# Kernel optimization log

Measured on AMD Instinct MI355X. Metric: run time of the kernel, lower is better.

Reference implementation:

```python
import jax, jax.numpy as jnp
import numpy as np

N_NODES = 100000
N_EDGES = 1200000
NUM_GRAPHS = 64
D_IN = 64
D_H = 64
D_OUT = 2
BN_EPS = 1e-5


def setup_inputs() -> dict:
    key = jax.random.key(0)
    ks = jax.random.split(key, 12)
    x = jax.random.normal(ks[0], (N_NODES, D_IN), dtype=jnp.float32)
    edge_index = jax.random.randint(ks[1], (2, N_EDGES), 0, N_NODES, dtype=jnp.int64 if jax.config.read('jax_enable_x64') else jnp.int32)
    batch = jnp.sort(jax.random.randint(ks[2], (N_NODES,), 0, NUM_GRAPHS))
    s = 1.0 / np.sqrt(D_H)
    W1 = jax.random.uniform(ks[3], (D_IN, D_H), minval=-s, maxval=s, dtype=jnp.float32)
    b1 = jnp.zeros((D_H,), jnp.float32)
    g1 = jnp.ones((D_H,), jnp.float32); be1 = jnp.zeros((D_H,), jnp.float32)
    m1 = jax.random.normal(ks[4], (D_H,), dtype=jnp.float32) * 0.1
    v1 = jax.random.uniform(ks[5], (D_H,), minval=0.5, maxval=1.5, dtype=jnp.float32)
    W2 = jax.random.uniform(ks[6], (D_H, D_H), minval=-s, maxval=s, dtype=jnp.float32)
    b2 = jnp.zeros((D_H,), jnp.float32)
    g2 = jnp.ones((D_H,), jnp.float32); be2 = jnp.zeros((D_H,), jnp.float32)
    m2 = jax.random.normal(ks[7], (D_H,), dtype=jnp.float32) * 0.1
    v2 = jax.random.uniform(ks[8], (D_H,), minval=0.5, maxval=1.5, dtype=jnp.float32)
    Wc = jax.random.uniform(ks[9], (D_H, D_OUT), minval=-s, maxval=s, dtype=jnp.float32)
    bc = jnp.zeros((D_OUT,), jnp.float32)
    return dict(x=x, edge_index=edge_index, batch=batch, W1=W1, b1=b1, g1=g1, be1=be1, m1=m1, v1=v1,
                W2=W2, b2=b2, g2=g2, be2=be2, m2=m2, v2=v2, Wc=Wc, bc=bc)


def _gcn_conv(x, src, dst, W, b):
    n = x.shape[0]
    h = x @ W  # [N, Dh]
    deg = jax.ops.segment_sum(jnp.ones_like(dst, dtype=h.dtype), dst, num_segments=n)  # includes self-loops
    dinv = jax.lax.rsqrt(jnp.maximum(deg, 1.0))
    norm = dinv[src] * dinv[dst]  # [E+N]
    msg = h[src] * norm[:, None]
    out = jax.ops.segment_sum(msg, dst, num_segments=n)
    return out + b


def _bn(x, g, be, m, v):
    return (x - m) * (g * jax.lax.rsqrt(v + BN_EPS)) + be


def reference(x, edge_index, batch, W1, b1, g1, be1, m1, v1, W2, b2, g2, be2, m2, v2, Wc, bc):
    n = x.shape[0]
    loop = jnp.arange(n, dtype=edge_index.dtype)
    src = jnp.concatenate([edge_index[0], loop])
    dst = jnp.concatenate([edge_index[1], loop])
    h = _gcn_conv(x, src, dst, W1, b1)
    h = jax.nn.relu(_bn(h, g1, be1, m1, v1))  # dropout is identity in eval
    h = _gcn_conv(h, src, dst, W2, b2)
    h = jax.nn.relu(_bn(h, g2, be2, m2, v2))
    # global mean pool over graphs
    sums = jax.ops.segment_sum(h, batch, num_segments=NUM_GRAPHS)
    cnts = jax.ops.segment_sum(jnp.ones((n,), h.dtype), batch, num_segments=NUM_GRAPHS)
    pooled = sums / jnp.maximum(cnts, 1.0)[:, None]
    return pooled @ Wc + bc
```

## Files before the change

kernel.cpp:

```cpp
#include <hip/hip_runtime.h>

#define N_NODES_C 100000
#define N_EDGES_C 1200000
#define NUM_GRAPHS_C 64
#define D_C 64
#define CAP_C 64
#define NPASS_C 8
#define BN_EPS_C 1e-5f

typedef unsigned short u16;
typedef unsigned int u32;

using frag_ab = __attribute__((ext_vector_type(8))) short;
using f32x4   = __attribute__((ext_vector_type(4))) float;

__device__ __forceinline__ u16 f2bf(float f) {
    u32 x = __float_as_uint(f);
    x += 0x7fffu + ((x >> 16) & 1u);
    return (u16)(x >> 16);
}
__device__ __forceinline__ float bf2f(u16 u) {
    return __uint_as_float(((u32)u) << 16);
}

__global__ void k_prep(const float* __restrict__ x,
                       const float* __restrict__ W1, const float* __restrict__ W2,
                       u16* __restrict__ Xb, u16* __restrict__ Wb1,
                       u16* __restrict__ Wb2, u16* __restrict__ T) {
    int i = blockIdx.x * 256 + threadIdx.x;
    int base = i * 4;
    if (base < N_NODES_C * D_C) {
        float4 f = *(const float4*)(x + base);
        ushort4 o;
        o.x = f2bf(f.x); o.y = f2bf(f.y); o.z = f2bf(f.z); o.w = f2bf(f.w);
        *(ushort4*)(Xb + base) = o;
    }
    if (i < 4096) {
        int n = i >> 6, k = i & 63;
        Wb1[i] = f2bf(W1[k * 64 + n]);
        Wb2[i] = f2bf(W2[k * 64 + n]);
    }
    if (i < 64) T[(size_t)N_NODES_C * 64 + i] = 0;
}

__global__ void __launch_bounds__(256) k_scatter(
        const int* __restrict__ src, const int* __restrict__ dst,
        int* __restrict__ cnt, int* __restrict__ col) {
    int pass = blockIdx.x & (NPASS_C - 1);
    int chunk = blockIdx.x >> 3;
    int nchunks = gridDim.x >> 3;
    const int RANGE = N_NODES_C / NPASS_C;
    int lo = pass * RANGE;
    int hi = (pass == NPASS_C - 1) ? N_NODES_C : lo + RANGE;
    const int nquads = N_EDGES_C / 4;
    int tid = chunk * 256 + threadIdx.x;
    int nthreads = nchunks * 256;
    const int4* dst4 = (const int4*)dst;
    const int4* src4 = (const int4*)src;
    for (int i = tid; i < nquads; i += nthreads) {
        int4 d4 = dst4[i];
        int dd[4] = {d4.x, d4.y, d4.z, d4.w};
        bool in0 = dd[0] >= lo && dd[0] < hi;
        bool in1 = dd[1] >= lo && dd[1] < hi;
        bool in2 = dd[2] >= lo && dd[2] < hi;
        bool in3 = dd[3] >= lo && dd[3] < hi;
        if (in0 | in1 | in2 | in3) {
            int4 s4 = src4[i];
            int ss[4] = {s4.x, s4.y, s4.z, s4.w};
            bool in[4] = {in0, in1, in2, in3};
#pragma unroll
            for (int k = 0; k < 4; ++k) {
                if (in[k]) {
                    int pos = atomicAdd(&cnt[dd[k]], 1);
                    if (pos < CAP_C) col[(size_t)dd[k] * CAP_C + pos] = ss[k];
                }
            }
        }
    }
}

__global__ void __launch_bounds__(256) k_gemm_mfma(
        const u16* __restrict__ Xb, const u16* __restrict__ Wb,
        const int* __restrict__ cnt, u16* __restrict__ T) {
    int lane = threadIdx.x & 63;
    int q = lane >> 4, ln = lane & 15;
    int wave = blockIdx.x * 4 + (threadIdx.x >> 6);
    int nwaves = gridDim.x * 4;
    frag_ab bfr[4][2];
#pragma unroll
    for (int nt = 0; nt < 4; ++nt)
#pragma unroll
        for (int kh = 0; kh < 2; ++kh)
            bfr[nt][kh] = *(const frag_ab*)(Wb + (nt * 16 + ln) * 64 + kh * 32 + q * 8);
    const int nstrips = N_NODES_C / 16;
    for (int s = wave; s < nstrips; s += nwaves) {
        int r0 = s * 16;
        frag_ab a0 = *(const frag_ab*)(Xb + (size_t)(r0 + ln) * 64 + q * 8);
        frag_ab a1 = *(const frag_ab*)(Xb + (size_t)(r0 + ln) * 64 + 32 + q * 8);
        f32x4 acc[4];
#pragma unroll
        for (int nt = 0; nt < 4; ++nt) {
            acc[nt] = (f32x4){0.f, 0.f, 0.f, 0.f};
            acc[nt] = __builtin_amdgcn_mfma_f32_16x16x32_bf16(a0, bfr[nt][0], acc[nt], 0, 0, 0);
            acc[nt] = __builtin_amdgcn_mfma_f32_16x16x32_bf16(a1, bfr[nt][1], acc[nt], 0, 0, 0);
        }
        float di[4];
#pragma unroll
        for (int reg = 0; reg < 4; ++reg)
            di[reg] = rsqrtf((float)(cnt[r0 + q * 4 + reg] + 1));
#pragma unroll
        for (int nt = 0; nt < 4; ++nt)
#pragma unroll
            for (int reg = 0; reg < 4; ++reg)
                T[(size_t)(r0 + q * 4 + reg) * 64 + nt * 16 + ln] =
                    f2bf(acc[nt][reg] * di[reg]);
    }
}

template <bool POOL>
__device__ __forceinline__ void gather_body(
        const u16* __restrict__ T, const int* __restrict__ col,
        const int* __restrict__ cnt,
        const float* __restrict__ b, const float* __restrict__ g,
        const float* __restrict__ be, const float* __restrict__ m,
        const float* __restrict__ v, const int* __restrict__ batch,
        u16* __restrict__ Ab, float* __restrict__ pooled) {
    const int ZROW = N_NODES_C;
    int lane = threadIdx.x & 63;
    int h = lane >> 4, c = lane & 15;
    int cbase = c << 2;
    int wave = blockIdx.x * 4 + (threadIdx.x >> 6);
    int nwaves = gridDim.x * 4;
    float scv[4], c0v[4];
#pragma unroll
    for (int i = 0; i < 4; ++i) {
        float sci = g[cbase + i] * rsqrtf(v[cbase + i] + BN_EPS_C);
        scv[i] = sci;
        c0v[i] = (b[cbase + i] - m[cbase + i]) * sci + be[cbase + i];
    }
    const int chunk = (N_NODES_C + nwaves - 1) / nwaves;
    int p0 = wave * chunk;
    int p1 = p0 + chunk; if (p1 > N_NODES_C) p1 = N_NODES_C;
    if (p0 >= p1) return;

    float psum = 0.f; int curg = -1;

    int dRaw = cnt[p0];
    int cvRaw = col[((size_t)(u32)p0 << 6) + lane];

    for (int p = p0; p < p1; ++p) {
        int deg = __builtin_amdgcn_readfirstlane(dRaw);
        if (deg > 63) deg = 63;
        int cvR = cvRaw;
        if (p + 1 < p1) {
            dRaw = cnt[p + 1];
            cvRaw = col[((size_t)(u32)(p + 1) << 6) + lane];
        }
        int cv = (lane < deg) ? cvR : ((lane == deg) ? p : ZROW);
        int iters = (deg + 4) >> 2;
        float a0 = 0.f, a1 = 0.f, a2 = 0.f, a3 = 0.f;
        int sl = h;
        int j = 0;
        for (; j + 2 <= iters; j += 2) {
            int i0 = __shfl(cv, sl);
            int i1 = __shfl(cv, sl + 4);
            uint2 t0 = *(const uint2*)(T + (((size_t)(u32)i0) << 6) + (c << 2));
            uint2 t1 = *(const uint2*)(T + (((size_t)(u32)i1) << 6) + (c << 2));
            a0 += __uint_as_float(t0.x << 16); a1 += __uint_as_float(t0.x & 0xffff0000u);
            a2 += __uint_as_float(t0.y << 16); a3 += __uint_as_float(t0.y & 0xffff0000u);
            a0 += __uint_as_float(t1.x << 16); a1 += __uint_as_float(t1.x & 0xffff0000u);
            a2 += __uint_as_float(t1.y << 16); a3 += __uint_as_float(t1.y & 0xffff0000u);
            sl += 8;
        }
        if (j < iters) {
            int i0 = __shfl(cv, sl);
            uint2 t0 = *(const uint2*)(T + (((size_t)(u32)i0) << 6) + (c << 2));
            a0 += __uint_as_float(t0.x << 16); a1 += __uint_as_float(t0.x & 0xffff0000u);
            a2 += __uint_as_float(t0.y << 16); a3 += __uint_as_float(t0.y & 0xffff0000u);
        }
        a0 += __shfl_xor(a0, 16); a0 += __shfl_xor(a0, 32);
        a1 += __shfl_xor(a1, 16); a1 += __shfl_xor(a1, 32);
        a2 += __shfl_xor(a2, 16); a2 += __shfl_xor(a2, 32);
        a3 += __shfl_xor(a3, 16); a3 += __shfl_xor(a3, 32);
        float dr = rsqrtf((float)(deg + 1));
        if (POOL) {
            float asel = (h & 2) ? ((h & 1) ? a3 : a2) : ((h & 1) ? a1 : a0);
            float scl  = (h & 2) ? ((h & 1) ? scv[3] : scv[2]) : ((h & 1) ? scv[1] : scv[0]);
            float c0l  = (h & 2) ? ((h & 1) ? c0v[3] : c0v[2]) : ((h & 1) ? c0v[1] : c0v[0]);
            float vh = fmaxf(fmaf(asel * dr, scl, c0l), 0.f);
            int gg = batch[p];
            if (gg != curg) {
                if (curg >= 0) atomicAdd(&pooled[curg * 64 + cbase + h], psum);
                curg = gg; psum = 0.f;
            }
            psum += vh;
        } else {
            float v0 = fmaxf(fmaf(a0 * dr, scv[0], c0v[0]), 0.f);
            float v1 = fmaxf(fmaf(a1 * dr, scv[1], c0v[1]), 0.f);
            float v2 = fmaxf(fmaf(a2 * dr, scv[2], c0v[2]), 0.f);
            float v3 = fmaxf(fmaf(a3 * dr, scv[3], c0v[3]), 0.f);
            if (h == 0) {
                u32 w0 = (u32)f2bf(v0) | ((u32)f2bf(v1) << 16);
                u32 w1 = (u32)f2bf(v2) | ((u32)f2bf(v3) << 16);
                *(uint2*)(Ab + (((size_t)(u32)p) << 6) + (c << 2)) = make_uint2(w0, w1);
            }
        }
    }
    if (POOL && curg >= 0) atomicAdd(&pooled[curg * 64 + cbase + h], psum);
}

__global__ void __launch_bounds__(256) k_gather1(
        const u16* __restrict__ T, const int* __restrict__ col,
        const int* __restrict__ cnt,
        const float* __restrict__ b, const float* __restrict__ g,
        const float* __restrict__ be, const float* __restrict__ m,
        const float* __restrict__ v, u16* __restrict__ Ab) {
    gather_body<false>(T, col, cnt, b, g, be, m, v, nullptr, Ab, nullptr);
}

__global__ void __launch_bounds__(256) k_gather2(
        const u16* __restrict__ T, const int* __restrict__ col,
        const int* __restrict__ cnt,
        const float* __restrict__ b, const float* __restrict__ g,
        const float* __restrict__ be, const float* __restrict__ m,
        const float* __restrict__ v, const int* __restrict__ batch,
        float* __restrict__ pooled) {
    gather_body<true>(T, col, cnt, b, g, be, m, v, batch, nullptr, pooled);
}

__global__ void k_final(const float* __restrict__ pooled, const int* __restrict__ batch,
                        const float* __restrict__ Wc, const float* __restrict__ bc,
                        float* __restrict__ out) {
    __shared__ float sp[64 * 65];
    __shared__ int sub[64];
    int t = threadIdx.x;
    for (int i = t; i < 4096; i += 256) sp[(i >> 6) * 65 + (i & 63)] = pooled[i];
    if (t < 64) {
        int lo = 0, hi = N_NODES_C;
        while (lo < hi) { int mid = (lo + hi) >> 1; if (batch[mid] > t) hi = mid; else lo = mid + 1; }
        sub[t] = lo;
    }
    __syncthreads();
    if (t < 64) {
        int gi = t;
        int lb = gi ? sub[gi - 1] : 0;
        int cntg = sub[gi] - lb;
        float inv = 1.0f / fmaxf((float)cntg, 1.0f);
        float a0 = 0.f, a1 = 0.f;
#pragma unroll 8
        for (int f = 0; f < 64; ++f) {
            float p = sp[gi * 65 + f];
            a0 = fmaf(p, Wc[f * 2 + 0], a0);
            a1 = fmaf(p, Wc[f * 2 + 1], a1);
        }
        out[gi * 2 + 0] = a0 * inv + bc[0];
        out[gi * 2 + 1] = a1 * inv + bc[1];
    }
}

extern "C" void kernel_launch(void* const* d_in, const int* in_sizes, int n_in,
                              void* d_out, int out_size, void* d_ws, size_t ws_size,
                              hipStream_t stream) {
    const float* x    = (const float*)d_in[0];
    const int*   ei   = (const int*)d_in[1];
    const int*   batch= (const int*)d_in[2];
    const float* W1 = (const float*)d_in[3];
    const float* b1 = (const float*)d_in[4];
    const float* g1 = (const float*)d_in[5];
    const float* be1= (const float*)d_in[6];
    const float* m1 = (const float*)d_in[7];
    const float* v1 = (const float*)d_in[8];
    const float* W2 = (const float*)d_in[9];
    const float* b2 = (const float*)d_in[10];
    const float* g2 = (const float*)d_in[11];
    const float* be2= (const float*)d_in[12];
    const float* m2 = (const float*)d_in[13];
    const float* v2 = (const float*)d_in[14];
    const float* Wc = (const float*)d_in[15];
    const float* bc = (const float*)d_in[16];
    float* out = (float*)d_out;

    char* ws = (char*)d_ws;
    size_t off = 0;
    auto alloc = [&](size_t bytes) {
        size_t o = off;
        off = (off + bytes + 511) & ~(size_t)511;
        return o;
    };
    size_t o_cnt   = alloc((size_t)N_NODES_C * 4);
    size_t o_pool  = alloc((size_t)NUM_GRAPHS_C * D_C * 4);
    size_t zero_bytes = off;
    size_t o_col   = alloc((size_t)N_NODES_C * CAP_C * 4);
    size_t o_xb    = alloc((size_t)N_NODES_C * D_C * 2);
    size_t o_wb1   = alloc(4096 * 2);
    size_t o_wb2   = alloc(4096 * 2);
    size_t o_t     = alloc((size_t)(N_NODES_C + 1) * D_C * 2);
    size_t o_ab    = alloc((size_t)N_NODES_C * D_C * 2);
    (void)ws_size; (void)in_sizes; (void)n_in; (void)out_size;

    int*   cnt    = (int*)(ws + o_cnt);
    float* pooled = (float*)(ws + o_pool);
    int*   col    = (int*)(ws + o_col);
    u16*   Xb     = (u16*)(ws + o_xb);
    u16*   Wb1    = (u16*)(ws + o_wb1);
    u16*   Wb2    = (u16*)(ws + o_wb2);
    u16*   T      = (u16*)(ws + o_t);
    u16*   Ab     = (u16*)(ws + o_ab);

    const int* srcp = ei;
    const int* dstp = ei + N_EDGES_C;

    hipMemsetAsync(ws, 0, zero_bytes, stream);

    int pblocks = (N_NODES_C * D_C / 4 + 255) / 256;
    int sblocks = 2048;
    int gblocks = 2048;
    int mblocks = 1563;
    k_prep<<<pblocks, 256, 0, stream>>>(x, W1, W2, Xb, Wb1, Wb2, T);
    k_scatter<<<sblocks, 256, 0, stream>>>(srcp, dstp, cnt, col);

    k_gemm_mfma<<<mblocks, 256, 0, stream>>>(Xb, Wb1, cnt, T);
    k_gather1<<<gblocks, 256, 0, stream>>>(T, col, cnt, b1, g1, be1, m1, v1, Ab);
    k_gemm_mfma<<<mblocks, 256, 0, stream>>>(Ab, Wb2, cnt, T);
    k_gather2<<<gblocks, 256, 0, stream>>>(T, col, cnt, b2, g2, be2, m2, v2,
                                           batch, pooled);
    k_final<<<1, 256, 0, stream>>>(pooled, batch, Wc, bc, out);
}
```

Baseline: 253.8 us.

## Replace fixed-capacity adjacency buckets with exact CSR built by count-scan-place

Swaps the padded per-node column buckets (64 slots each) for a compact CSR layout. Degrees and per-edge slot positions are counted with atomics in the prep kernel, a three-kernel prefix scan gives row starts, and a placement kernel writes sources without atomics. Gather kernels read neighbour lists from the CSR offsets, which shrinks the column array and makes reads contiguous. In exchange it adds three scan launches plus the pos array traffic, and the placement step still does scattered writes.

```diff
diff --git a/kernel.cpp b/kernel.cpp
--- a/kernel.cpp
+++ b/kernel.cpp
@@ -4,9 +4,9 @@
 #define N_EDGES_C 1200000
 #define NUM_GRAPHS_C 64
 #define D_C 64
-#define CAP_C 64
 #define NPASS_C 8
 #define BN_EPS_C 1e-5f
+#define SCAN_B 391
 
 typedef unsigned short u16;
 typedef unsigned int u32;
@@ -25,8 +25,10 @@
 
 __global__ void k_prep(const float* __restrict__ x,
                        const float* __restrict__ W1, const float* __restrict__ W2,
+                       const int* __restrict__ dst,
                        u16* __restrict__ Xb, u16* __restrict__ Wb1,
-                       u16* __restrict__ Wb2, u16* __restrict__ T) {
+                       u16* __restrict__ Wb2, u16* __restrict__ T,
+                       int* __restrict__ cnt, int* __restrict__ pos) {
     int i = blockIdx.x * 256 + threadIdx.x;
     int base = i * 4;
     if (base < N_NODES_C * D_C) {
@@ -41,11 +43,62 @@
         Wb2[i] = f2bf(W2[k * 64 + n]);
     }
     if (i < 64) T[(size_t)N_NODES_C * 64 + i] = 0;
-}
-
-__global__ void __launch_bounds__(256) k_scatter(
+    if (i < N_EDGES_C) {
+        int d = dst[i];
+        pos[i] = atomicAdd(&cnt[d], 1);
+    }
+}
+
+__global__ void __launch_bounds__(256) k_scan1(const int* __restrict__ cnt,
+                                               int* __restrict__ start,
+                                               int* __restrict__ bsum) {
+    __shared__ int sh[256];
+    int t = threadIdx.x;
+    int i = blockIdx.x * 256 + t;
+    int c = (i < N_NODES_C) ? cnt[i] : 0;
+    int val = c;
+    sh[t] = val;
+    __syncthreads();
+#pragma unroll
+    for (int off = 1; off < 256; off <<= 1) {
+        int y = (t >= off) ? sh[t - off] : 0;
+        __syncthreads();
+        val += y;
+        sh[t] = val;
+        __syncthreads();
+    }
+    if (i < N_NODES_C) start[i] = val - c;
+    if (t == 255) bsum[blockIdx.x] = val;
+}
+
+__global__ void __launch_bounds__(512) k_scan2(int* __restrict__ bsum) {
+    __shared__ int sh[512];
+    int t = threadIdx.x;
+    int c = (t < SCAN_B) ? bsum[t] : 0;
+    int val = c;
+    sh[t] = val;
+    __syncthreads();
+#pragma unroll
+    for (int off = 1; off < 512; off <<= 1) {
+        int y = (t >= off) ? sh[t - off] : 0;
+        __syncthreads();
+        val += y;
+        sh[t] = val;
+        __syncthreads();
+    }
+    if (t < SCAN_B) bsum[t] = val - c;
+}
+
+__global__ void __launch_bounds__(256) k_scan3(int* __restrict__ start,
+                                               const int* __restrict__ bsum) {
+    int i = blockIdx.x * 256 + threadIdx.x;
+    if (i < N_NODES_C) start[i] += bsum[blockIdx.x];
+}
+
+__global__ void __launch_bounds__(256) k_place(
         const int* __restrict__ src, const int* __restrict__ dst,
-        int* __restrict__ cnt, int* __restrict__ col) {
+        const int* __restrict__ pos, const int* __restrict__ start,
+        int* __restrict__ col) {
     int pass = blockIdx.x & (NPASS_C - 1);
     int chunk = blockIdx.x >> 3;
     int nchunks = gridDim.x >> 3;
@@ -57,6 +110,7 @@
     int nthreads = nchunks * 256;
     const int4* dst4 = (const int4*)dst;
     const int4* src4 = (const int4*)src;
+    const int4* pos4 = (const int4*)pos;
     for (int i = tid; i < nquads; i += nthreads) {
         int4 d4 = dst4[i];
         int dd[4] = {d4.x, d4.y, d4.z, d4.w};
@@ -66,13 +120,14 @@
         bool in3 = dd[3] >= lo && dd[3] < hi;
         if (in0 | in1 | in2 | in3) {
             int4 s4 = src4[i];
+            int4 p4 = pos4[i];
             int ss[4] = {s4.x, s4.y, s4.z, s4.w};
+            int pp[4] = {p4.x, p4.y, p4.z, p4.w};
             bool in[4] = {in0, in1, in2, in3};
 #pragma unroll
             for (int k = 0; k < 4; ++k) {
                 if (in[k]) {
-                    int pos = atomicAdd(&cnt[dd[k]], 1);
-                    if (pos < CAP_C) col[(size_t)dd[k] * CAP_C + pos] = ss[k];
+                    col[(size_t)(u32)(start[dd[k]] + pp[k])] = ss[k];
                 }
             }
         }
@@ -120,7 +175,7 @@
 template <bool POOL>
 __device__ __forceinline__ void gather_body(
         const u16* __restrict__ T, const int* __restrict__ col,
-        const int* __restrict__ cnt,
+        const int* __restrict__ cnt, const int* __restrict__ start,
         const float* __restrict__ b, const float* __restrict__ g,
         const float* __restrict__ be, const float* __restrict__ m,
         const float* __restrict__ v, const int* __restrict__ batch,
@@ -145,17 +200,21 @@
 
     float psum = 0.f; int curg = -1;
 
-    int dRaw = cnt[p0];
-    int cvRaw = col[((size_t)(u32)p0 << 6) + lane];
+    int d0 = cnt[p0];
+    int s0 = start[p0];
+    int d1 = 0, s1 = 0;
+    if (p0 + 1 < p1) { d1 = cnt[p0 + 1]; s1 = start[p0 + 1]; }
+    int cv0 = col[(size_t)(u32)s0 + lane];
 
     for (int p = p0; p < p1; ++p) {
-        int deg = __builtin_amdgcn_readfirstlane(dRaw);
+        int deg = __builtin_amdgcn_readfirstlane(d0);
+        int cvR = cv0;
+        if (p + 1 < p1) {
+            cv0 = col[(size_t)(u32)s1 + lane];
+            d0 = d1;
+            if (p + 2 < p1) { d1 = cnt[p + 2]; s1 = start[p + 2]; }
+        }
         if (deg > 63) deg = 63;
-        int cvR = cvRaw;
-        if (p + 1 < p1) {
-            dRaw = cnt[p + 1];
-            cvRaw = col[((size_t)(u32)(p + 1) << 6) + lane];
-        }
         int cv = (lane < deg) ? cvR : ((lane == deg) ? p : ZROW);
         int iters = (deg + 4) >> 2;
         float a0 = 0.f, a1 = 0.f, a2 = 0.f, a3 = 0.f;
@@ -211,21 +270,21 @@
 
 __global__ void __launch_bounds__(256) k_gather1(
         const u16* __restrict__ T, const int* __restrict__ col,
-        const int* __restrict__ cnt,
+        const int* __restrict__ cnt, const int* __restrict__ start,
         const float* __restrict__ b, const float* __restrict__ g,
         const float* __restrict__ be, const float* __restrict__ m,
         const float* __restrict__ v, u16* __restrict__ Ab) {
-    gather_body<false>(T, col, cnt, b, g, be, m, v, nullptr, Ab, nullptr);
+    gather_body<false>(T, col, cnt, start, b, g, be, m, v, nullptr, Ab, nullptr);
 }
 
 __global__ void __launch_bounds__(256) k_gather2(
         const u16* __restrict__ T, const int* __restrict__ col,
-        const int* __restrict__ cnt,
+        const int* __restrict__ cnt, const int* __restrict__ start,
         const float* __restrict__ b, const float* __restrict__ g,
         const float* __restrict__ be, const float* __restrict__ m,
         const float* __restrict__ v, const int* __restrict__ batch,
         float* __restrict__ pooled) {
-    gather_body<true>(T, col, cnt, b, g, be, m, v, batch, nullptr, pooled);
+    gather_body<true>(T, col, cnt, start, b, g, be, m, v, batch, nullptr, pooled);
 }
 
 __global__ void k_final(const float* __restrict__ pooled, const int* __restrict__ batch,
@@ -290,7 +349,10 @@
     size_t o_cnt   = alloc((size_t)N_NODES_C * 4);
     size_t o_pool  = alloc((size_t)NUM_GRAPHS_C * D_C * 4);
     size_t zero_bytes = off;
-    size_t o_col   = alloc((size_t)N_NODES_C * CAP_C * 4);
+    size_t o_col   = alloc((size_t)(N_EDGES_C + 64) * 4);
+    size_t o_pos   = alloc((size_t)N_EDGES_C * 4);
+    size_t o_start = alloc((size_t)(N_NODES_C + 64) * 4);
+    size_t o_bsum  = alloc(512 * 4);
     size_t o_xb    = alloc((size_t)N_NODES_C * D_C * 2);
     size_t o_wb1   = alloc(4096 * 2);
     size_t o_wb2   = alloc(4096 * 2);
@@ -301,6 +363,9 @@
     int*   cnt    = (int*)(ws + o_cnt);
     float* pooled = (float*)(ws + o_pool);
     int*   col    = (int*)(ws + o_col);
+    int*   pos    = (int*)(ws + o_pos);
+    int*   startp = (int*)(ws + o_start);
+    int*   bsum   = (int*)(ws + o_bsum);
     u16*   Xb     = (u16*)(ws + o_xb);
     u16*   Wb1    = (u16*)(ws + o_wb1);
     u16*   Wb2    = (u16*)(ws + o_wb2);
@@ -316,13 +381,16 @@
     int sblocks = 2048;
     int gblocks = 2048;
     int mblocks = 1563;
-    k_prep<<<pblocks, 256, 0, stream>>>(x, W1, W2, Xb, Wb1, Wb2, T);
-    k_scatter<<<sblocks, 256, 0, stream>>>(srcp, dstp, cnt, col);
+    k_prep<<<pblocks, 256, 0, stream>>>(x, W1, W2, dstp, Xb, Wb1, Wb2, T, cnt, pos);
+    k_scan1<<<SCAN_B, 256, 0, stream>>>(cnt, startp, bsum);
+    k_scan2<<<1, 512, 0, stream>>>(bsum);
+    k_scan3<<<SCAN_B, 256, 0, stream>>>(startp, bsum);
+    k_place<<<sblocks, 256, 0, stream>>>(srcp, dstp, pos, startp, col);
 
     k_gemm_mfma<<<mblocks, 256, 0, stream>>>(Xb, Wb1, cnt, T);
-    k_gather1<<<gblocks, 256, 0, stream>>>(T, col, cnt, b1, g1, be1, m1, v1, Ab);
+    k_gather1<<<gblocks, 256, 0, stream>>>(T, col, cnt, startp, b1, g1, be1, m1, v1, Ab);
     k_gemm_mfma<<<mblocks, 256, 0, stream>>>(Ab, Wb2, cnt, T);
-    k_gather2<<<gblocks, 256, 0, stream>>>(T, col, cnt, b2, g2, be2, m2, v2,
+    k_gather2<<<gblocks, 256, 0, stream>>>(T, col, cnt, startp, b2, g2, be2, m2, v2,
                                            batch, pooled);
     k_final<<<1, 256, 0, stream>>>(pooled, batch, Wc, bc, out);
 }
```

Result: slower. 272.2 us (+7.3%).
